# Performance work log

Hardware: AMD Instinct MI355X
Metric: run time of the kernel (lower is better)

Reference implementation:

```python
import jax, jax.numpy as jnp
import numpy as np

NINP, NHID, K = 300, 64, 2   # input dim, hidden dim, pyramid levels (from Net.__init__)
GH = NHID // K               # per-pyramid-level width contributed to each gate (32)
S, B = 512, 256              # seq_len, batch


def setup_inputs() -> dict:
    key = jax.random.key(0)
    k = jax.random.split(key, 5)
    s = 0.05
    return {
        "x": jax.random.normal(k[0], (S, B, NINP), jnp.float32),
        "h0": jnp.zeros((B, NHID), jnp.float32),
        "c0": jnp.zeros((B, NHID), jnp.float32),
        "W_pt0": jax.random.normal(k[1], (NINP, 4 * GH), jnp.float32) * s,
        "b_pt0": jnp.zeros((4 * GH,), jnp.float32),
        "W_pt1": jax.random.normal(k[2], (NINP // 2, 4 * GH), jnp.float32) * s,
        "b_pt1": jnp.zeros((4 * GH,), jnp.float32),
        "W_glt": jax.random.normal(k[3], (1, NHID, 4 * NHID), jnp.float32) * s,  # g=1 grouped linear
        "W_dec": jax.random.normal(k[4], (NHID, 3), jnp.float32) * s,
        "b_dec": jnp.zeros((3,), jnp.float32),
    }


def _pyramidal_i2h(x, W_pt0, b_pt0, W_pt1, b_pt1):
    # Pyramidal transform: level 0 = full-res input, level 1 = features avg-pooled by 2.
    # Each level produces 4*GH gate features; levels are concatenated per gate -> NHID.
    x1 = x.reshape(x.shape[0], x.shape[1], NINP // 2, 2).mean(-1)  # (S,B,150)
    g0 = (x @ W_pt0 + b_pt0).reshape(x.shape[0], x.shape[1], 4, GH)
    g1 = (x1 @ W_pt1 + b_pt1).reshape(x.shape[0], x.shape[1], 4, GH)
    return jnp.concatenate([g0, g1], axis=-1)  # (S,B,4,NHID) gates order: f,g,i,o


def reference(x, h0, c0, W_pt0, b_pt0, W_pt1, b_pt1, W_glt, W_dec, b_dec):
    # Precompute input-to-hidden gate contributions for all timesteps (same math as per-step).
    i2h = _pyramidal_i2h(x, W_pt0, b_pt0, W_pt1, b_pt1)  # (S,B,4,NHID)
    bsz = h0.shape[0]

    def step(carry, i2h_t):
        h, c = carry
        # grouped linear (g=1): (B,1,NHID) x (1,NHID,4*NHID) -> (B,4,NHID)
        h2h = jnp.einsum('bgi,gio->bgo', h.reshape(bsz, 1, NHID), W_glt).reshape(bsz, 4, NHID)
        gates = i2h_t + h2h
        f, g, i, o = gates[:, 0], gates[:, 1], gates[:, 2], gates[:, 3]
        c1 = jax.nn.sigmoid(f) * c + jax.nn.sigmoid(i) * jnp.tanh(g)
        h1 = jax.nn.sigmoid(o) * jnp.tanh(c1)
        return (h1, c1), h1

    (hT, cT), hs = jax.lax.scan(step, (h0, c0), i2h)  # hs: (S,B,NHID)
    decoded = hs @ W_dec + b_dec                       # (S,B,3)
    return decoded, hT, cT
```

## Files before the change

### kernel.cpp

```cpp
#include <hip/hip_runtime.h>
#include <hip/hip_bf16.h>

#define SLEN 512
#define BATCH 256
#define NIN 300
#define KP 320
#define NG 256
#define NH 64
#define BM 128
#define BN 128
#define BK 64
#define LDP 72
#define TC 128
#define NCH (SLEN / TC)

typedef float f32x4 __attribute__((ext_vector_type(4)));
typedef _Float16 f16x8 __attribute__((ext_vector_type(8)));
typedef _Float16 f16x4 __attribute__((ext_vector_type(4)));

__global__ void prep_w(const float* __restrict__ Wpt0, const float* __restrict__ bpt0,
                       const float* __restrict__ Wpt1, const float* __restrict__ bpt1,
                       const float* __restrict__ Wglt,
                       _Float16* __restrict__ Wc16, float* __restrict__ bcat,
                       _Float16* __restrict__ Wg16) {
  int idx = blockIdx.x * 256 + threadIdx.x;
  if (idx < NG * KP) {
    int n = idx / KP, k = idx - n * KP;
    int g = n >> 6, h = n & 63;
    float w = 0.f;
    if (k < NIN) {
      if (h < 32) w = Wpt0[k * 128 + g * 32 + h];
      else        w = 0.5f * Wpt1[(k >> 1) * 128 + g * 32 + (h - 32)];
    }
    Wc16[idx] = (_Float16)w;
  }
  if (idx < NG * NH) {
    int c = idx >> 6, k = idx & 63;
    Wg16[idx] = (_Float16)Wglt[k * NG + c];
  }
  if (idx < NG) {
    int g = idx >> 6, h = idx & 63;
    bcat[idx] = (h < 32) ? bpt0[g * 32 + h] : bpt1[g * 32 + h - 32];
  }
}


__device__ __forceinline__ void gemm_body(
    char* LB, int m0, int n0, int tid,
    const float* __restrict__ x, const _Float16* __restrict__ Wc16,
    const float* __restrict__ bcat, _Float16* __restrict__ C) {
  _Float16 (*As)[LDP] = reinterpret_cast<_Float16(*)[LDP]>(LB);
  _Float16 (*Bs)[LDP] = reinterpret_cast<_Float16(*)[LDP]>(LB + BM * LDP * 2);
  const int lane = tid & 63;
  const int w = tid >> 6;
  const int wr = w >> 1, wc = w & 1;

  f32x4 acc[4][4];
#pragma unroll
  for (int m = 0; m < 4; ++m)
#pragma unroll
    for (int n = 0; n < 4; ++n) acc[m][n] = (f32x4){0.f, 0.f, 0.f, 0.f};

  const int arow_l = tid >> 4;
  const int acol   = (tid & 15) * 4;
  const int brow_l = tid >> 3;
  const int bcol   = (tid & 7) * 8;

  for (int k0 = 0; k0 < KP; k0 += BK) {
#pragma unroll
    for (int p = 0; p < 8; ++p) {
      int row = p * 16 + arow_l;
      int gk = k0 + acol;
      f32x4 v = (f32x4){0.f, 0.f, 0.f, 0.f};
      if (gk + 3 < NIN)
        v = *reinterpret_cast<const f32x4*>(&x[(size_t)(m0 + row) * NIN + gk]);
      f16x4 sv;
      sv[0] = (_Float16)v[0]; sv[1] = (_Float16)v[1];
      sv[2] = (_Float16)v[2]; sv[3] = (_Float16)v[3];
      *reinterpret_cast<f16x4*>(&As[row][acol]) = sv;
    }
#pragma unroll
    for (int p = 0; p < 4; ++p) {
      int n = p * 32 + brow_l;
      f16x8 v = *reinterpret_cast<const f16x8*>(&Wc16[(size_t)(n0 + n) * KP + k0 + bcol]);
      *reinterpret_cast<f16x8*>(&Bs[n][bcol]) = v;
    }
    __syncthreads();
#pragma unroll
    for (int ks = 0; ks < 2; ++ks) {
      const int kk = ks * 32 + (lane >> 4) * 8;
      f16x8 a[4], b[4];
#pragma unroll
      for (int m = 0; m < 4; ++m)
        a[m] = *reinterpret_cast<const f16x8*>(&As[wr * 64 + m * 16 + (lane & 15)][kk]);
#pragma unroll
      for (int n = 0; n < 4; ++n)
        b[n] = *reinterpret_cast<const f16x8*>(&Bs[wc * 64 + n * 16 + (lane & 15)][kk]);
#pragma unroll
      for (int m = 0; m < 4; ++m)
#pragma unroll
        for (int n = 0; n < 4; ++n)
          acc[m][n] = __builtin_amdgcn_mfma_f32_16x16x32_f16(a[m], b[n], acc[m][n], 0, 0, 0);
    }
    __syncthreads();
  }
  const int fc = lane & 15;
  const int fr = (lane >> 4) * 4;
#pragma unroll
  for (int n = 0; n < 4; ++n) {
    int col = n0 + wc * 64 + n * 16 + fc;
    float bias = bcat[col];
#pragma unroll
    for (int m = 0; m < 4; ++m) {
#pragma unroll
      for (int r = 0; r < 4; ++r) {
        int row = m0 + wr * 64 + m * 16 + fr + r;
        C[(size_t)row * NG + col] = (_Float16)(acc[m][n][r] + bias);
      }
    }
  }
}

__device__ __forceinline__ void decode_body(
    char* LB, int blk, int tid,
    const _Float16* __restrict__ hs, const float* __restrict__ Wdec,
    const float* __restrict__ bdec, float* __restrict__ out) {
  float* wl = reinterpret_cast<float*>(LB);
  float* bl = reinterpret_cast<float*>(LB + 768);
  float* ob = reinterpret_cast<float*>(LB + 784);
  if (tid < NH * 3) wl[tid] = Wdec[tid];
  if (tid < 3) bl[tid] = bdec[tid];
  __syncthreads();
  const size_t idx = (size_t)blk * 256 + tid;
  const _Float16* hp = hs + idx * NH;
  float d0 = 0.f, d1 = 0.f, d2 = 0.f;
#pragma unroll
  for (int k = 0; k < NH; k += 8) {
    f16x8 h8 = *reinterpret_cast<const f16x8*>(&hp[k]);
#pragma unroll
    for (int j = 0; j < 8; ++j) {
      float hv = (float)h8[j];
      d0 += hv * wl[(k + j) * 3 + 0];
      d1 += hv * wl[(k + j) * 3 + 1];
      d2 += hv * wl[(k + j) * 3 + 2];
    }
  }
  ob[tid * 3 + 0] = d0 + bl[0];
  ob[tid * 3 + 1] = d1 + bl[1];
  ob[tid * 3 + 2] = d2 + bl[2];
  __syncthreads();
  if (tid < 192) {
    f32x4* o4 = reinterpret_cast<f32x4*>(out + (size_t)blk * 768);
    o4[tid] = reinterpret_cast<const f32x4*>(ob)[tid];
  }
}

#define PAIR(v, j) __builtin_shufflevector(v, v, 2*(j), 2*(j)+1)
#define DOT(hb, i, W) { f16x8 hv = (hb)[i]; \
      acc0 = __builtin_amdgcn_fdot2(PAIR(hv,0), PAIR(W,0), acc0, false); \
      acc1 = __builtin_amdgcn_fdot2(PAIR(hv,1), PAIR(W,1), acc1, false); \
      acc0 = __builtin_amdgcn_fdot2(PAIR(hv,2), PAIR(W,2), acc0, false); \
      acc1 = __builtin_amdgcn_fdot2(PAIR(hv,3), PAIR(W,3), acc1, false); }

#define STEP(CUR, SP) { \
    float cur_ = (float)__builtin_bit_cast(_Float16, (unsigned short)(CUR)); \
    const f16x8* hb = reinterpret_cast<const f16x8*>(hbuf + ((SP) & 1) * NH); \
    float acc0 = 0.f, acc1 = 0.f; \
    DOT(hb, 0, w0) DOT(hb, 1, w1) DOT(hb, 2, w2) DOT(hb, 3, w3) \
    DOT(hb, 4, w4) DOT(hb, 5, w5) DOT(hb, 6, w6) DOT(hb, 7, w7) \
    float pre = cur_ + (acc0 + acc1); \
    float xx = fminf(fmaxf(pre, -30.f), 30.f); \
    float e = __expf(-mm * xx); \
    float y = 1.f / (1.f + e); \
    float act = (g == 1) ? (2.f * y - 1.f) : y; \
    float g_ = __shfl(act, l + 16); \
    float i_ = __shfl(act, l + 32); \
    float o_ = __shfl(act, l + 48); \
    if (l < 16) { \
      float c1 = act * creg + i_ * g_; \
      creg = c1; \
      float ct = fminf(fmaxf(c1, -15.f), 15.f); \
      float e2 = __expf(-2.f * ct); \
      float th = (1.f - e2) / (1.f + e2); \
      float h1 = o_ * th; \
      hreg = h1; \
      hbuf[(((SP) + 1) & 1) * NH + hidx] = (_Float16)h1; \
      *hp = (_Float16)h1;   \
    } \
    hp += st >> 2;  \
    asm volatile("s_waitcnt lgkmcnt(0)" ::: "memory"); \
    __builtin_amdgcn_s_barrier(); }


__global__ __launch_bounds__(256, 2) void gemm_i2h(
    const float* __restrict__ x, const _Float16* __restrict__ Wc16,
    const float* __restrict__ bcat, _Float16* __restrict__ C) {
  __shared__ __align__(16) char LB[36864];
  gemm_body(LB, blockIdx.y * BM, blockIdx.x * BN, threadIdx.x, x, Wc16, bcat, C);
}

__global__ __launch_bounds__(256) void decode(
    const _Float16* __restrict__ hs, const float* __restrict__ Wdec,
    const float* __restrict__ bdec, float* __restrict__ out) {
  __shared__ __align__(16) char LB[4096];
  decode_body(LB, blockIdx.x, threadIdx.x, hs, Wdec, bdec, out);
}

__global__ __launch_bounds__(256, 2)
void fused_step(
    const _Float16* __restrict__ i2h_cur, _Float16* __restrict__ i2h_next,
    const float* __restrict__ x_next,
    const _Float16* __restrict__ Wc16, const float* __restrict__ bcat,
    const _Float16* __restrict__ Wg16,
    const float* __restrict__ h_in, const float* __restrict__ c_in,
    float* __restrict__ h_state, float* __restrict__ c_state,
    _Float16* __restrict__ hs_cur, const _Float16* __restrict__ hs_prev,
    const float* __restrict__ Wdec, const float* __restrict__ bdec,
    float* __restrict__ out_prev,
    float* __restrict__ hT_out, float* __restrict__ cT_out,
    int is_last, int has_gemm) {
  __shared__ __align__(16) char LB[36864];
  const int bid = blockIdx.x;
  const int tid = threadIdx.x;

  if (bid < BATCH) {
    const int b = bid;
    const int ww = tid >> 6;
    const int l = tid & 63;
    const int g = l >> 4;
    const int hidx = ww * 16 + (l & 15);
    const int col = g * 64 + hidx;

    f16x8* Wst = reinterpret_cast<f16x8*>(LB);
    _Float16* hbuf = reinterpret_cast<_Float16*>(LB);

    for (int e = tid; e < 8 * NG; e += 256) {
      int kk = e >> 8, c = e & 255;
      Wst[e] = *reinterpret_cast<const f16x8*>(Wg16 + (size_t)c * NH + kk * 8);
    }
    __syncthreads();

    f16x8 w0 = Wst[0 * NG + col], w1 = Wst[1 * NG + col];
    f16x8 w2 = Wst[2 * NG + col], w3 = Wst[3 * NG + col];
    f16x8 w4 = Wst[4 * NG + col], w5 = Wst[5 * NG + col];
    f16x8 w6 = Wst[6 * NG + col], w7 = Wst[7 * NG + col];

    float creg = 0.f, hreg = 0.f;
    if (l < 16) creg = c_in[b * NH + hidx];
    float h0v = (tid < NH) ? h_in[b * NH + tid] : 0.f;
    __syncthreads();

    if (tid < NH) hbuf[tid] = (_Float16)h0v;
    __syncthreads();

    const size_t st = (size_t)NG * BATCH;
    const unsigned short* ip =
        reinterpret_cast<const unsigned short*>(i2h_cur) + (size_t)b * NG + col;
    _Float16* hp = hs_cur + (size_t)b * NH + hidx;
    const float mm = (g == 1) ? 2.f : 1.f;

    int s = 0;
    {
      unsigned short c0v = ip[0],      c1v = ip[st],     c2v = ip[2 * st], c3v = ip[3 * st];
      unsigned short n0v = ip[4 * st], n1v = ip[5 * st], n2v = ip[6 * st], n3v = ip[7 * st];
      const unsigned short* ipf = ip + 8 * st;
      while (s + 4 <= TC) {
        unsigned short f0v = 0, f1v = 0, f2v = 0, f3v = 0;
        if (s + 8  < TC) f0v = ipf[0];
        if (s + 9  < TC) f1v = ipf[st];
        if (s + 10 < TC) f2v = ipf[2 * st];
        if (s + 11 < TC) f3v = ipf[3 * st];
        ipf += 4 * st;
        STEP(c0v, s)
        STEP(c1v, s + 1)
        STEP(c2v, s + 2)
        STEP(c3v, s + 3)
        c0v = n0v; c1v = n1v; c2v = n2v; c3v = n3v;
        n0v = f0v; n1v = f1v; n2v = f2v; n3v = f3v;
        s += 4;
      }
    }

    if (l < 16) {
      h_state[b * NH + hidx] = hreg;
      c_state[b * NH + hidx] = creg;
      if (is_last) {
        hT_out[b * NH + hidx] = hreg;
        cT_out[b * NH + hidx] = creg;
      }
    }
  } else if (has_gemm && bid < BATCH + 2 * (TC * BATCH / BM)) {
    const int gid = bid - BATCH;
    const int n0 = (gid & 1) * BN;
    const int m0 = (gid >> 1) * BM;
    gemm_body(LB, m0, n0, tid, x_next, Wc16, bcat, i2h_next);
  } else {
    const int did = bid - BATCH - (has_gemm ? 2 * (TC * BATCH / BM) : 0);
    decode_body(LB, did, tid, hs_prev, Wdec, bdec, out_prev);
  }
}

extern "C" void kernel_launch(void* const* d_in, const int* in_sizes, int n_in,
                              void* d_out, int out_size, void* d_ws, size_t ws_size,
                              hipStream_t stream) {
  const float* x    = (const float*)d_in[0];
  const float* h0   = (const float*)d_in[1];
  const float* c0   = (const float*)d_in[2];
  const float* Wpt0 = (const float*)d_in[3];
  const float* bpt0 = (const float*)d_in[4];
  const float* Wpt1 = (const float*)d_in[5];
  const float* bpt1 = (const float*)d_in[6];
  const float* Wglt = (const float*)d_in[7];
  const float* Wdec = (const float*)d_in[8];
  const float* bdec = (const float*)d_in[9];
  float* out = (float*)d_out;

  char* ws = (char*)d_ws;
  _Float16*  Wc16    = (_Float16*)(ws);
  float*     bcat    = (float*)(ws + 163840);
  _Float16*  Wg16    = (_Float16*)(ws + 164864);
  float*     h_state = (float*)(ws + 197632);
  float*     c_state = (float*)(ws + 263168);
  const size_t base = 328704;

  const size_t chunk_i2h = (size_t)TC * BATCH * NG;
  _Float16* i2h0 = (_Float16*)(ws + base);
  _Float16* i2h1 = i2h0 + chunk_i2h;
  _Float16* hs   = (_Float16*)(ws + base + 4 * chunk_i2h);

  prep_w<<<dim3((NG * KP + 255) / 256), dim3(256), 0, stream>>>(
      Wpt0, bpt0, Wpt1, bpt1, Wglt, Wc16, bcat, Wg16);

  gemm_i2h<<<dim3(2, TC * BATCH / BM), dim3(256), 0, stream>>>(
      x, Wc16, bcat, i2h0);

  for (int k = 0; k < NCH; ++k) {
    _Float16* cur = (k & 1) ? i2h1 : i2h0;
    _Float16* nxt = (k & 1) ? i2h0 : i2h1;
    const int has_gemm = (k + 1 < NCH) ? 1 : 0;
    const int has_dec  = (k > 0) ? 1 : 0;
    const int nblk = BATCH + (has_gemm ? 2 * (TC * BATCH / BM) : 0)
                           + (has_dec ? (TC * BATCH / 256) : 0);
    const int kp = (k > 0) ? (k - 1) : 0;
    fused_step<<<dim3(nblk), dim3(256), 0, stream>>>(
        cur, nxt, x + (size_t)(k + 1) * TC * BATCH * NIN,
        Wc16, bcat, Wg16,
        (k == 0) ? h0 : h_state, (k == 0) ? c0 : c_state,
        h_state, c_state,
        hs + (size_t)k * TC * BATCH * NH,
        hs + (size_t)kp * TC * BATCH * NH,
        Wdec, bdec,
        out + (size_t)kp * TC * BATCH * 3,
        out + (size_t)SLEN * BATCH * 3,
        out + (size_t)SLEN * BATCH * 3 + BATCH * NH,
        (k == NCH - 1) ? 1 : 0, has_gemm);
  }

  decode<<<dim3(TC * BATCH / 256), dim3(256), 0, stream>>>(
      hs + (size_t)(NCH - 1) * TC * BATCH * NH, Wdec, bdec,
      out + (size_t)(NCH - 1) * TC * BATCH * 3);
}
```

Before: 276.9 us.

## Compute all four gates per lane in one wave, dropping shuffles and barriers

The recurrent block now uses a single 64-lane wave per batch element. Each lane holds the weights for all four gates of one hidden unit and computes f, g, i and o itself, so the per-step cross-lane shuffles and block-wide barriers disappear. The GEMM epilogue writes i2h with the gate dimension interleaved, so each lane fetches its four gate pre-activations with one 4x16-bit load. The cost is four times more dot-product work and register pressure per lane on the serial critical path. It also uses an approximate reciprocal in the activations.

Result: slower. 310.1 us (+12.0%).

```diff
diff --git a/kernel.cpp b/kernel.cpp
--- a/kernel.cpp
+++ b/kernel.cpp
@@ -17,6 +17,7 @@
 typedef float f32x4 __attribute__((ext_vector_type(4)));
 typedef _Float16 f16x8 __attribute__((ext_vector_type(8)));
 typedef _Float16 f16x4 __attribute__((ext_vector_type(4)));
+typedef unsigned short u16x4 __attribute__((ext_vector_type(4)));
 
 __global__ void prep_w(const float* __restrict__ Wpt0, const float* __restrict__ bpt0,
                        const float* __restrict__ Wpt1, const float* __restrict__ bpt1,
@@ -109,13 +110,14 @@
 #pragma unroll
   for (int n = 0; n < 4; ++n) {
     int col = n0 + wc * 64 + n * 16 + fc;
+    int nidx = ((col & 63) << 2) | (col >> 6);
     float bias = bcat[col];
 #pragma unroll
     for (int m = 0; m < 4; ++m) {
 #pragma unroll
       for (int r = 0; r < 4; ++r) {
         int row = m0 + wr * 64 + m * 16 + fr + r;
-        C[(size_t)row * NG + col] = (_Float16)(acc[m][n][r] + bias);
+        C[(size_t)row * NG + nidx] = (_Float16)(acc[m][n][r] + bias);
       }
     }
   }
@@ -156,40 +158,50 @@
 }
 
 #define PAIR(v, j) __builtin_shufflevector(v, v, 2*(j), 2*(j)+1)
-#define DOT(hb, i, W) { f16x8 hv = (hb)[i]; \
-      acc0 = __builtin_amdgcn_fdot2(PAIR(hv,0), PAIR(W,0), acc0, false); \
-      acc1 = __builtin_amdgcn_fdot2(PAIR(hv,1), PAIR(W,1), acc1, false); \
-      acc0 = __builtin_amdgcn_fdot2(PAIR(hv,2), PAIR(W,2), acc0, false); \
-      acc1 = __builtin_amdgcn_fdot2(PAIR(hv,3), PAIR(W,3), acc1, false); }
-
-#define STEP(CUR, SP) { \
-    float cur_ = (float)__builtin_bit_cast(_Float16, (unsigned short)(CUR)); \
-    const f16x8* hb = reinterpret_cast<const f16x8*>(hbuf + ((SP) & 1) * NH); \
-    float acc0 = 0.f, acc1 = 0.f; \
-    DOT(hb, 0, w0) DOT(hb, 1, w1) DOT(hb, 2, w2) DOT(hb, 3, w3) \
-    DOT(hb, 4, w4) DOT(hb, 5, w5) DOT(hb, 6, w6) DOT(hb, 7, w7) \
-    float pre = cur_ + (acc0 + acc1); \
-    float xx = fminf(fmaxf(pre, -30.f), 30.f); \
-    float e = __expf(-mm * xx); \
-    float y = 1.f / (1.f + e); \
-    float act = (g == 1) ? (2.f * y - 1.f) : y; \
-    float g_ = __shfl(act, l + 16); \
-    float i_ = __shfl(act, l + 32); \
-    float o_ = __shfl(act, l + 48); \
-    if (l < 16) { \
-      float c1 = act * creg + i_ * g_; \
-      creg = c1; \
-      float ct = fminf(fmaxf(c1, -15.f), 15.f); \
-      float e2 = __expf(-2.f * ct); \
-      float th = (1.f - e2) / (1.f + e2); \
-      float h1 = o_ * th; \
-      hreg = h1; \
-      hbuf[(((SP) + 1) & 1) * NH + hidx] = (_Float16)h1; \
-      *hp = (_Float16)h1;   \
-    } \
-    hp += st >> 2;  \
-    asm volatile("s_waitcnt lgkmcnt(0)" ::: "memory"); \
-    __builtin_amdgcn_s_barrier(); }
+#define ACT1(SD, X, MUL, CL) { \
+    float xx_ = fminf(fmaxf((X), -(CL)), (CL)); \
+    float ee_ = __expf(-(MUL) * xx_); \
+    SD = __builtin_amdgcn_rcpf(1.f + ee_); }
+
+#define DOTCH(KK) { f16x8 hv = hb[KK]; \
+    aF0 = __builtin_amdgcn_fdot2(PAIR(hv,0), PAIR(wF##KK,0), aF0, false); \
+    aG0 = __builtin_amdgcn_fdot2(PAIR(hv,0), PAIR(wG##KK,0), aG0, false); \
+    aI0 = __builtin_amdgcn_fdot2(PAIR(hv,0), PAIR(wI##KK,0), aI0, false); \
+    aO0 = __builtin_amdgcn_fdot2(PAIR(hv,0), PAIR(wO##KK,0), aO0, false); \
+    aF1 = __builtin_amdgcn_fdot2(PAIR(hv,1), PAIR(wF##KK,1), aF1, false); \
+    aG1 = __builtin_amdgcn_fdot2(PAIR(hv,1), PAIR(wG##KK,1), aG1, false); \
+    aI1 = __builtin_amdgcn_fdot2(PAIR(hv,1), PAIR(wI##KK,1), aI1, false); \
+    aO1 = __builtin_amdgcn_fdot2(PAIR(hv,1), PAIR(wO##KK,1), aO1, false); \
+    aF0 = __builtin_amdgcn_fdot2(PAIR(hv,2), PAIR(wF##KK,2), aF0, false); \
+    aG0 = __builtin_amdgcn_fdot2(PAIR(hv,2), PAIR(wG##KK,2), aG0, false); \
+    aI0 = __builtin_amdgcn_fdot2(PAIR(hv,2), PAIR(wI##KK,2), aI0, false); \
+    aO0 = __builtin_amdgcn_fdot2(PAIR(hv,2), PAIR(wO##KK,2), aO0, false); \
+    aF1 = __builtin_amdgcn_fdot2(PAIR(hv,3), PAIR(wF##KK,3), aF1, false); \
+    aG1 = __builtin_amdgcn_fdot2(PAIR(hv,3), PAIR(wG##KK,3), aG1, false); \
+    aI1 = __builtin_amdgcn_fdot2(PAIR(hv,3), PAIR(wI##KK,3), aI1, false); \
+    aO1 = __builtin_amdgcn_fdot2(PAIR(hv,3), PAIR(wO##KK,3), aO1, false); }
+
+#define STEP(CURV) { \
+    float pF = (float)__builtin_bit_cast(_Float16, (unsigned short)(CURV)[0]); \
+    float pG = (float)__builtin_bit_cast(_Float16, (unsigned short)(CURV)[1]); \
+    float pI = (float)__builtin_bit_cast(_Float16, (unsigned short)(CURV)[2]); \
+    float pO = (float)__builtin_bit_cast(_Float16, (unsigned short)(CURV)[3]); \
+    const f16x8* hb = reinterpret_cast<const f16x8*>(hbuf); \
+    float aF0 = 0.f, aF1 = 0.f, aG0 = 0.f, aG1 = 0.f; \
+    float aI0 = 0.f, aI1 = 0.f, aO0 = 0.f, aO1 = 0.f; \
+    DOTCH(0) DOTCH(1) DOTCH(2) DOTCH(3) DOTCH(4) DOTCH(5) DOTCH(6) DOTCH(7) \
+    pF += aF0 + aF1; pG += aG0 + aG1; pI += aI0 + aI1; pO += aO0 + aO1; \
+    float sF, sG2, sI, sO; \
+    ACT1(sF, pF, 1.f, 30.f) ACT1(sG2, pG, 2.f, 15.f) \
+    ACT1(sI, pI, 1.f, 30.f) ACT1(sO, pO, 1.f, 30.f) \
+    float tG = 2.f * sG2 - 1.f; \
+    float c1 = sF * creg + sI * tG; creg = c1; \
+    float sT2; ACT1(sT2, c1, 2.f, 15.f) \
+    float th = 2.f * sT2 - 1.f; \
+    float h1 = sO * th; hreg = h1; \
+    hbuf[l] = (_Float16)h1;               \
+    *hp = (_Float16)h1; hp += (size_t)BATCH * NH;   \
+    asm volatile("s_waitcnt lgkmcnt(0)" ::: "memory"); }
 
 
 __global__ __launch_bounds__(256, 2) void gemm_i2h(
@@ -225,69 +237,61 @@
 
   if (bid < BATCH) {
     const int b = bid;
-    const int ww = tid >> 6;
     const int l = tid & 63;
-    const int g = l >> 4;
-    const int hidx = ww * 16 + (l & 15);
-    const int col = g * 64 + hidx;
 
     f16x8* Wst = reinterpret_cast<f16x8*>(LB);
-    _Float16* hbuf = reinterpret_cast<_Float16*>(LB);
+    unsigned hoff = 0;
+    asm volatile("" : "+s"(hoff));
+    _Float16* hbuf = reinterpret_cast<_Float16*>(LB + hoff);
 
     for (int e = tid; e < 8 * NG; e += 256) {
       int kk = e >> 8, c = e & 255;
       Wst[e] = *reinterpret_cast<const f16x8*>(Wg16 + (size_t)c * NH + kk * 8);
     }
     __syncthreads();
-
-    f16x8 w0 = Wst[0 * NG + col], w1 = Wst[1 * NG + col];
-    f16x8 w2 = Wst[2 * NG + col], w3 = Wst[3 * NG + col];
-    f16x8 w4 = Wst[4 * NG + col], w5 = Wst[5 * NG + col];
-    f16x8 w6 = Wst[6 * NG + col], w7 = Wst[7 * NG + col];
-
-    float creg = 0.f, hreg = 0.f;
-    if (l < 16) creg = c_in[b * NH + hidx];
-    float h0v = (tid < NH) ? h_in[b * NH + tid] : 0.f;
-    __syncthreads();
-
-    if (tid < NH) hbuf[tid] = (_Float16)h0v;
-    __syncthreads();
-
-    const size_t st = (size_t)NG * BATCH;
-    const unsigned short* ip =
-        reinterpret_cast<const unsigned short*>(i2h_cur) + (size_t)b * NG + col;
-    _Float16* hp = hs_cur + (size_t)b * NH + hidx;
-    const float mm = (g == 1) ? 2.f : 1.f;
+    if (tid >= 64) return;
+
+#define LW(G, N, KK) f16x8 w##N##KK = Wst[(KK) * NG + (G) * 64 + l];
+#define LWROW(G, N) LW(G,N,0) LW(G,N,1) LW(G,N,2) LW(G,N,3) LW(G,N,4) LW(G,N,5) LW(G,N,6) LW(G,N,7)
+    LWROW(0, F) LWROW(1, G) LWROW(2, I) LWROW(3, O)
+
+    float creg = c_in[b * NH + l];
+    float hreg = h_in[b * NH + l];
+    hbuf[l] = (_Float16)hreg;
+    asm volatile("s_waitcnt lgkmcnt(0)" ::: "memory");
+
+    const size_t S4 = (size_t)NG * BATCH / 4;
+    const u16x4* ip = reinterpret_cast<const u16x4*>(
+        reinterpret_cast<const unsigned short*>(i2h_cur) + (size_t)b * NG) + l;
+    _Float16* hp = hs_cur + (size_t)b * NH + l;
 
     int s = 0;
     {
-      unsigned short c0v = ip[0],      c1v = ip[st],     c2v = ip[2 * st], c3v = ip[3 * st];
-      unsigned short n0v = ip[4 * st], n1v = ip[5 * st], n2v = ip[6 * st], n3v = ip[7 * st];
-      const unsigned short* ipf = ip + 8 * st;
+      u16x4 c0v = ip[0],      c1v = ip[S4],     c2v = ip[2 * S4], c3v = ip[3 * S4];
+      u16x4 n0v = ip[4 * S4], n1v = ip[5 * S4], n2v = ip[6 * S4], n3v = ip[7 * S4];
+      const u16x4* ipf = ip + 8 * S4;
       while (s + 4 <= TC) {
-        unsigned short f0v = 0, f1v = 0, f2v = 0, f3v = 0;
+        u16x4 f0v = (u16x4){0, 0, 0, 0}, f1v = f0v, f2v = f0v, f3v = f0v;
         if (s + 8  < TC) f0v = ipf[0];
-        if (s + 9  < TC) f1v = ipf[st];
-        if (s + 10 < TC) f2v = ipf[2 * st];
-        if (s + 11 < TC) f3v = ipf[3 * st];
-        ipf += 4 * st;
-        STEP(c0v, s)
-        STEP(c1v, s + 1)
-        STEP(c2v, s + 2)
-        STEP(c3v, s + 3)
+        if (s + 9  < TC) f1v = ipf[S4];
+        if (s + 10 < TC) f2v = ipf[2 * S4];
+        if (s + 11 < TC) f3v = ipf[3 * S4];
+        ipf += 4 * S4;
+        STEP(c0v)
+        STEP(c1v)
+        STEP(c2v)
+        STEP(c3v)
         c0v = n0v; c1v = n1v; c2v = n2v; c3v = n3v;
         n0v = f0v; n1v = f1v; n2v = f2v; n3v = f3v;
         s += 4;
       }
     }
 
-    if (l < 16) {
-      h_state[b * NH + hidx] = hreg;
-      c_state[b * NH + hidx] = creg;
-      if (is_last) {
-        hT_out[b * NH + hidx] = hreg;
-        cT_out[b * NH + hidx] = creg;
-      }
+    h_state[b * NH + l] = hreg;
+    c_state[b * NH + l] = creg;
+    if (is_last) {
+      hT_out[b * NH + l] = hreg;
+      cT_out[b * NH + l] = creg;
     }
   } else if (has_gemm && bid < BATCH + 2 * (TC * BATCH / BM)) {
     const int gid = bid - BATCH;
```
